# Performance work log

Hardware: AMD Instinct MI355X
Metric: run time of the kernel (lower is better)

The kernel has to match this reference:

```python
import jax, jax.numpy as jnp
import numpy as np

DIM, M_DIM, FOURIER, KNN = 128, 16, 4, 32
EDGE_IN = 2 * FOURIER + 2 * DIM + 1  # 265


def silu(x):
    return x * jax.nn.sigmoid(x)


def setup_inputs() -> dict:
    key = jax.random.key(0)
    ks = jax.random.split(key, 12)
    b, n = 2, 4096

    def w(k, shape):
        return jax.random.normal(k, shape, dtype=jnp.float32) * 0.02

    return {
        "feats": jax.random.normal(ks[0], (b, n, DIM), dtype=jnp.float32),
        "coors": jax.random.normal(ks[1], (b, n, 3), dtype=jnp.float32) * 3.0,
        # edge_mlp: Linear(265, 530) -> SiLU -> Linear(530, 16) -> SiLU
        "We1": w(ks[2], (EDGE_IN, 2 * EDGE_IN)), "be1": jnp.zeros((2 * EDGE_IN,), jnp.float32),
        "We2": w(ks[3], (2 * EDGE_IN, M_DIM)), "be2": jnp.zeros((M_DIM,), jnp.float32),
        # coors_mlp: Linear(16, 64) -> SiLU -> Linear(64, 1)
        "Wc1": w(ks[4], (M_DIM, 4 * M_DIM)), "bc1": jnp.zeros((4 * M_DIM,), jnp.float32),
        "Wc2": w(ks[5], (4 * M_DIM, 1)), "bc2": jnp.zeros((1,), jnp.float32),
        # node_mlp: Linear(dim+16, 2*dim) -> SiLU -> Linear(2*dim, dim)
        "Wn1": w(ks[6], (DIM + M_DIM, 2 * DIM)), "bn1": jnp.zeros((2 * DIM,), jnp.float32),
        "Wn2": w(ks[7], (2 * DIM, DIM)), "bn2": jnp.zeros((DIM,), jnp.float32),
    }


def reference(feats, coors, We1, be1, We2, be2, Wc1, bc1, Wc2, bc2, Wn1, bn1, Wn2, bn2):
    b, n, d = feats.shape
    # pairwise relative coords and squared distance: (b, n, n, 3), (b, n, n)
    rel_coors = coors[:, :, None, :] - coors[:, None, :, :]
    rel_dist = jnp.sum(rel_coors ** 2, axis=-1)

    # k nearest neighbors (smallest distance)
    _, idx = jax.lax.top_k(-rel_dist, KNN)  # (b, n, K)
    rel_coors = jnp.take_along_axis(rel_coors, idx[..., None], axis=2)  # (b, n, K, 3)
    rel_dist = jnp.take_along_axis(rel_dist, idx, axis=2)[..., None]    # (b, n, K, 1)

    # fourier encode distance -> (b, n, K, 2*F + 1)
    scales = 2.0 ** jnp.arange(FOURIER, dtype=rel_dist.dtype)
    xs = rel_dist[..., None] / scales  # (b, n, K, 1, F)
    fe = jnp.concatenate([jnp.sin(xs), jnp.cos(xs), rel_dist[..., None]], axis=-1)
    rel_dist = fe.reshape(b, n, KNN, 2 * FOURIER + 1)

    bidx = jnp.arange(b)[:, None, None]
    feats_j = feats[bidx, idx]                                   # (b, n, K, d)
    feats_i = jnp.broadcast_to(feats[:, :, None, :], (b, n, KNN, d))

    edge_in = jnp.concatenate([feats_i, feats_j, rel_dist], axis=-1)  # (b, n, K, 265)
    m_ij = silu(silu(edge_in @ We1 + be1) @ We2 + be2)                # (b, n, K, m)

    coor_w = (silu(m_ij @ Wc1 + bc1) @ Wc2 + bc2)[..., 0]             # (b, n, K)
    coors_out = jnp.einsum('bij,bijc->bic', coor_w, rel_coors) + coors

    m_i = m_ij.sum(axis=2)                                            # (b, n, m)
    node_h = silu(jnp.concatenate([feats, m_i], axis=-1) @ Wn1 + bn1)
    node_out = node_h @ Wn2 + bn2 + feats
    return node_out, coors_out
```

## Files before the change

kernel.cpp:

```cpp
#include <hip/hip_runtime.h>
#include <hip/hip_bf16.h>
#include <stdint.h>

typedef __hip_bfloat16 bf16;

using sh8    = __attribute__((ext_vector_type(8)))  short;
using sh4    = __attribute__((ext_vector_type(4)))  short;
using us4    = __attribute__((ext_vector_type(4)))  unsigned short;
using f32x16 = __attribute__((ext_vector_type(16))) float;
using fx4    = __attribute__((ext_vector_type(4)))  float;

#define NN    4096
#define NODES 8192
#define DIM   128
#define MD    16
#define KNNK  32
#define H1N   530
#define CPAD  544
#define PROW  1088

#define OFF_W1AB 0
#define OFF_WE2A 8704
#define OFF_WC1A 17536
#define OFF_BE2  19584
#define OFF_BC1  19616
#define OFF_WC2  19744
#define OFF_BC2  19872
#define WIMG_SH  19880

__device__ __forceinline__ float b2f(bf16 x){ return __bfloat162float(x); }
__device__ __forceinline__ bf16  f2b(float x){ return __float2bfloat16(x); }
__device__ __forceinline__ float silu_f(float x){
    return x * __builtin_amdgcn_rcpf(1.f + __expf(-x));
}

__device__ __forceinline__ unsigned short f2us(float f){
    unsigned x = __float_as_uint(f);
    unsigned r = x + 0x7FFFu + ((x >> 16) & 1u);
    return (unsigned short)(r >> 16);
}
__device__ __forceinline__ float us2f(unsigned short u){
    return __uint_as_float(((unsigned)u) << 16);
}
__device__ __forceinline__ unsigned pkbf(float a, float b){
    __hip_bfloat162 v = __float22bfloat162_rn(make_float2(a, b));
    return *(unsigned*)&v;
}

struct Ptrs { const void* p[14]; int n[14]; };

__global__ __launch_bounds__(256) void detect_kernel(Ptrs ps, int* flags){
    int tn = blockIdx.x;
    const bf16* s = (const bf16*)ps.p[tn];
    int n = ps.n[tn]; if (n > 8192) n = 8192;
    int bad = 0;
    for (int i = threadIdx.x; i < n; i += 256){
        float v = b2f(s[i]);
        if (!(fabsf(v) <= 64.f)) bad = 1;
    }
    __shared__ int sbad;
    if (threadIdx.x == 0) sbad = 0;
    __syncthreads();
    if (bad) atomicOr(&sbad, 1);
    __syncthreads();
    if (threadIdx.x == 0) flags[tn] = sbad;
}

struct ConvTab {
    const void* src[14];
    int dstoff[14];
    int prefix[15];
};

__global__ __launch_bounds__(256) void convert_all(ConvTab tab,
                                                   const int* __restrict__ flags,
                                                   float* __restrict__ base){
    int gid = blockIdx.x * 256 + threadIdx.x;
    if (gid >= tab.prefix[14]) return;
    int tn = 0;
    #pragma unroll
    for (int k = 1; k < 14; ++k)
        if (gid >= tab.prefix[k]) tn = k;
    int local = gid - tab.prefix[tn];
    int f = flags[tn];
    float v = f ? ((const float*)tab.src[tn])[local]
                : b2f(((const bf16*)tab.src[tn])[local]);
    base[tab.dstoff[tn] + local] = v;
}

__global__ __launch_bounds__(256) void prep_kernel(
        const float* __restrict__ We1, const float* __restrict__ We2,
        const float* __restrict__ Wc1, const float* __restrict__ be2,
        const float* __restrict__ bc1, const float* __restrict__ Wc2,
        const float* __restrict__ bc2, const float* __restrict__ feats,
        unsigned short* __restrict__ gwimg,
        unsigned short* __restrict__ We1T,
        unsigned short* __restrict__ fBF){
    int gid = blockIdx.x * 256 + threadIdx.x;
    if (gid < 4352){
        int c = gid >> 3, f = gid & 7;
        gwimg[OFF_W1AB + gid] = (c < H1N) ? f2us(We1[(size_t)(256 + f) * H1N + c]) : 0;
    } else if (gid < 8704){
        int e = gid - 4352; int c = e >> 3, jj = e & 7;
        gwimg[OFF_W1AB + 4352 + e] =
            (jj == 0 && c < H1N) ? f2us(We1[(size_t)264 * H1N + c]) : 0;
    } else if (gid < 17536){
        int e = gid - 8704; int o = e / 552, c = e - o * 552;
        gwimg[OFF_WE2A + e] = (c < H1N) ? f2us(We2[(size_t)c * 16 + o]) : 0;
    } else if (gid < 19584){
        int e = gid - 17536; int u = e >> 5, k = e & 31;
        gwimg[OFF_WC1A + e] = (k < 16) ? f2us(Wc1[(size_t)k * 64 + u]) : 0;
    } else if (gid < 19600){
        ((float*)(gwimg + OFF_BE2))[gid - 19584] = be2[gid - 19584];
    } else if (gid < 19664){
        ((float*)(gwimg + OFF_BC1))[gid - 19600] = bc1[gid - 19600];
    } else if (gid < 19728){
        ((float*)(gwimg + OFF_WC2))[gid - 19664] = Wc2[gid - 19664];
    } else if (gid < 19732){
        int z = gid - 19728;
        ((float*)(gwimg + OFF_BC2))[z] = (z == 0) ? bc2[0] : 0.f;
    } else if (gid >= 32768 && gid < 32768 + 1088 * 128){
        int e = gid - 32768; int n = e >> 7, k = e & 127;
        float v;
        if (n < CPAD) v = (n < H1N) ? We1[(size_t)k * H1N + n] : 0.f;
        else { int n2 = n - CPAD; v = (n2 < H1N) ? We1[(size_t)(128 + k) * H1N + n2] : 0.f; }
        We1T[e] = f2us(v);
    } else if (gid >= 172032 && gid < 172032 + NODES * DIM){
        int e = gid - 172032;
        fBF[e] = f2us(feats[e]);
    }
}

__global__ __launch_bounds__(512, 6) void knn_kernel(const float* __restrict__ coors,
                                                     int* __restrict__ idx_out){
    __shared__ unsigned hist[8][1024];
    __shared__ unsigned long long blist[8][64];
    __shared__ int cntO[8], cntB[8];

    int t = threadIdx.x, lane = t & 63, wid = t >> 6;
    int node = (blockIdx.x << 3) + wid;
    int b = node >> 12, i = node & (NN - 1);
    const float* cb = coors + (size_t)b * NN * 3;

    float qx = cb[i*3+0], qy = cb[i*3+1], qz = cb[i*3+2];

    unsigned* h = &hist[wid][0];
    {
        uint4* hz = (uint4*)h;
        uint4 z = make_uint4(0,0,0,0);
        #pragma unroll
        for (int zl = 0; zl < 4; ++zl) hz[zl * 64 + lane] = z;
    }
    if (lane == 0){ cntO[wid] = 0; cntB[wid] = 0; }
    asm volatile("" ::: "memory");

    #pragma unroll 4
    for (int s = 0; s < 64; ++s){
        int j = (s << 6) + lane;
        float dx = qx - cb[j*3+0];
        float dy = qy - cb[j*3+1];
        float dz = qz - cb[j*3+2];
        float d  = dx*dx + dy*dy + dz*dz;
        float d2 = d * d;
        atomicAdd(&h[__float_as_uint(d2 * d2) >> 22], 1u);
    }
    asm volatile("s_waitcnt lgkmcnt(0)" ::: "memory");

    unsigned S = 0;
    {
        uint4* hz = (uint4*)h;
        #pragma unroll
        for (int g = 0; g < 4; ++g){
            uint4 v = hz[lane * 4 + g];
            S += v.x + v.y + v.z + v.w;
        }
    }
    unsigned scan = S;
    #pragma unroll
    for (int off = 1; off < 64; off <<= 1){
        unsigned nv = __shfl_up(scan, off);
        if (lane >= off) scan += nv;
    }
    unsigned excl = scan - S;
    unsigned long long own = __ballot(excl < KNNK && excl + S >= KNNK);
    int src = __ffsll((unsigned long long)own) - 1;
    unsigned run = excl, Bloc = 0, below_l = 0;
    #pragma unroll
    for (int r = 0; r < 16; ++r){
        unsigned c = h[lane * 16 + r];
        if (run < KNNK && run + c >= KNNK){ Bloc = lane * 16 + r; below_l = run; }
        run += c;
    }
    unsigned B    = __shfl(Bloc, src);
    unsigned below= __shfl(below_l, src);
    unsigned need = KNNK - below;

    int* co = &cntO[wid];
    int* cbn = &cntB[wid];
    unsigned long long* bl = &blist[wid][0];
    #pragma unroll 4
    for (int s = 0; s < 64; ++s){
        int j = (s << 6) + lane;
        float dx = qx - cb[j*3+0];
        float dy = qy - cb[j*3+1];
        float dz = qz - cb[j*3+2];
        float d  = dx*dx + dy*dy + dz*dz;
        float d2 = d * d;
        unsigned bk = __float_as_uint(d2 * d2) >> 22;
        if (bk < B){
            int pos = atomicAdd(co, 1);
            idx_out[(size_t)node * KNNK + pos] = j;
        } else if (bk == B){
            unsigned long long mk = ((unsigned long long)__float_as_uint(d) << 32)
                                    | (unsigned)j;
            int p = atomicAdd(cbn, 1);
            if (p < 64) bl[p] = mk;
        }
    }
    asm volatile("s_waitcnt lgkmcnt(0) vmcnt(0)" ::: "memory");
    int nb = *cbn;

    if (nb <= 64){
        unsigned long long e = (lane < nb) ? bl[lane] : ~0ull;
        for (unsigned r = 0; r < need; ++r){
            unsigned long long m = e;
            #pragma unroll
            for (int off = 32; off > 0; off >>= 1){
                unsigned long long o = __shfl_xor(m, off);
                if (o < m) m = o;
            }
            if (lane == 0)
                idx_out[(size_t)node * KNNK + below + r] = (int)(unsigned)(m & 0xffffffffull);
            if (e == m) e = ~0ull;
        }
    } else {
        unsigned long long lastk = 0;
        for (unsigned r = 0; r < need; ++r){
            unsigned long long lmin = ~0ull;
            for (int s = 0; s < 64; ++s){
                int j = (s << 6) + lane;
                float dx = qx - cb[j*3+0];
                float dy = qy - cb[j*3+1];
                float dz = qz - cb[j*3+2];
                float d  = dx*dx + dy*dy + dz*dz;
                float d2 = d * d;
                if ((__float_as_uint(d2 * d2) >> 22) == B){
                    unsigned long long mk = (((unsigned long long)__float_as_uint(d) << 32)
                                             | (unsigned)j) + 1ull;
                    if (mk > lastk && mk < lmin) lmin = mk;
                }
            }
            #pragma unroll
            for (int off = 32; off > 0; off >>= 1){
                unsigned long long o = __shfl_xor(lmin, off);
                if (o < lmin) lmin = o;
            }
            if (lane == 0)
                idx_out[(size_t)node * KNNK + below + r] =
                    (int)(unsigned)((lmin - 1ull) & 0xffffffffull);
            lastk = lmin;
        }
    }
}

__global__ __launch_bounds__(256) void p_gemm(const unsigned short* __restrict__ fBF,
                                              const unsigned short* __restrict__ We1T,
                                              const float* __restrict__ be1,
                                              unsigned short* __restrict__ P){
    int t = threadIdx.x, lane = t & 63, wid = t >> 6;
    int e31 = lane & 31, hi = lane >> 5;
    int mW = (blockIdx.x << 7) + (wid << 5);
    int n0 = blockIdx.y << 5;

    const unsigned short* Arow = fBF  + (size_t)(mW + e31) * DIM + hi * 8;
    const unsigned short* Brow = We1T + (size_t)(n0 + e31) * DIM + hi * 8;

    f32x16 acc = {0.f,0.f,0.f,0.f,0.f,0.f,0.f,0.f,0.f,0.f,0.f,0.f,0.f,0.f,0.f,0.f};
    #pragma unroll
    for (int kc = 0; kc < 8; ++kc){
        sh8 a  = *(const sh8*)(Arow + kc * 16);
        sh8 bv = *(const sh8*)(Brow + kc * 16);
        acc = __builtin_amdgcn_mfma_f32_32x32x16_bf16(a, bv, acc, 0, 0, 0);
    }
    int n = n0 + e31;
    float beadd = 0.f;
    if (n < CPAD) beadd = (n < H1N) ? be1[n] : 0.f;
    #pragma unroll
    for (int g = 0; g < 4; ++g)
        #pragma unroll
        for (int r = 0; r < 4; ++r){
            int m = mW + 8*g + 4*hi + r;
            P[(size_t)m * PROW + n] = f2us(acc[4*g + r] + beadd);
        }
}

__global__ __launch_bounds__(512, 6) void edge_kernel(
        const float* __restrict__ coors, const int* __restrict__ idx,
        const unsigned short* __restrict__ gw,
        const unsigned short* __restrict__ P,
        float* __restrict__ mi_out, void* __restrict__ dout,
        const int* __restrict__ flagp){
    __shared__ __align__(16) unsigned short sWe2[16 * 552];
    __shared__ __align__(16) unsigned short trans[8][1280];

    int t = threadIdx.x, lane = t & 63, wid = t >> 6;
    int gnode = (blockIdx.x << 3) + wid;
    int b = gnode >> 12;

    {
        const float4* s1 = (const float4*)(gw + OFF_WE2A);
        float4* d1 = (float4*)sWe2;
        for (int e = t; e < 1104; e += 512) d1[e] = s1[e];
    }

    const float* cb = coors + (size_t)b * NN * 3;
    int i = gnode & (NN - 1);
    float qx = cb[i*3+0], qy = cb[i*3+1], qz = cb[i*3+2];

    int e31 = lane & 31, hi = lane >> 5;
    int e15 = lane & 15, q  = lane >> 4;

    int jme = idx[(size_t)gnode * KNNK + e31];
    float rx = qx - cb[jme*3+0];
    float ry = qy - cb[jme*3+1];
    float rz = qz - cb[jme*3+2];
    float d = rx*rx + ry*ry + rz*rz;

    unsigned frb[9];
    frb[0] = f2us(sinf(d));         frb[1] = f2us(sinf(d * 0.5f));
    frb[2] = f2us(sinf(d * 0.25f)); frb[3] = f2us(sinf(d * 0.125f));
    frb[4] = f2us(cosf(d));         frb[5] = f2us(cosf(d * 0.5f));
    frb[6] = f2us(cosf(d * 0.25f)); frb[7] = f2us(cosf(d * 0.125f));
    frb[8] = f2us(d);

    sh8 bfragC;
    #pragma unroll
    for (int j = 0; j < 8; ++j)
        bfragC[j] = (hi == 0) ? (short)frb[j]
                  : (short)((j == 0) ? frb[8] : (j == 1) ? 0x3F80u : 0u);

    int nbase = gnode & ~(NN - 1);
    int j0 = __shfl(jme, lane >> 2);
    int j1 = __shfl(jme, 16 + (lane >> 2));
    const unsigned short* Pst0 = P + (size_t)(nbase + j0) * PROW + CPAD + (lane & 3) * 8;
    const unsigned short* Pst1 = P + (size_t)(nbase + j1) * PROW + CPAD + (lane & 3) * 8;
    const unsigned short* Pirow = P + (size_t)gnode * PROW;

    unsigned short* stg = &trans[wid][0];
    unsigned short* sw0 = stg + (lane >> 2) * 40 + (lane & 3) * 8;
    unsigned short* sw1 = stg + (16 + (lane >> 2)) * 40 + (lane & 3) * 8;

    const float* g_be2 = (const float*)(gw + OFF_BE2);
    const float* g_bc1 = (const float*)(gw + OFF_BC1);
    const float* g_wc2 = (const float*)(gw + OFF_WC2);
    const float* g_bc2 = (const float*)(gw + OFF_BC2);

    fx4 accD0 = {0.f,0.f,0.f,0.f};
    fx4 accD1 = {0.f,0.f,0.f,0.f};

    __syncthreads();

    for (int ch = 0; ch < 17; ++ch){
        int c0 = ch * 32;
        sh8 g0v = *(const sh8*)(Pst0 + c0);
        sh8 g1v = *(const sh8*)(Pst1 + c0);
        unsigned short piS = Pirow[c0 + e31];
        sh8 afrag = *(const sh8*)(gw + OFF_W1AB + (size_t)(hi * 544 + c0 + e31) * 8);
        afrag[1] = hi ? (short)piS : afrag[1];

        *(sh8*)sw0 = g0v;
        *(sh8*)sw1 = g1v;
        asm volatile("s_waitcnt lgkmcnt(0)" ::: "memory");

        f32x16 cc;
        #pragma unroll
        for (int g = 0; g < 4; ++g){
            us4 pj = *(const us4*)(stg + e31 * 40 + 8*g + 4*hi);
            cc[4*g+0] = us2f(pj.x);
            cc[4*g+1] = us2f(pj.y);
            cc[4*g+2] = us2f(pj.z);
            cc[4*g+3] = us2f(pj.w);
        }
        f32x16 h = __builtin_amdgcn_mfma_f32_32x32x16_bf16(afrag, bfragC, cc, 0, 0, 0);

        #pragma unroll
        for (int g = 0; g < 4; ++g){
            unsigned lo = pkbf(silu_f(h[4*g+0]), silu_f(h[4*g+1]));
            unsigned hi2 = pkbf(silu_f(h[4*g+2]), silu_f(h[4*g+3]));
            *(uint2*)&stg[e31 * 40 + 8*g + 4*hi] = make_uint2(lo, hi2);
        }
        asm volatile("s_waitcnt lgkmcnt(0)" ::: "memory");

        sh8 wa  = *(const sh8*)&sWe2[e15 * 552 + c0 + q * 8];
        sh8 bt0 = *(const sh8*)&stg[e15 * 40 + q * 8];
        sh8 bt1 = *(const sh8*)&stg[(16 + e15) * 40 + q * 8];
        accD0 = __builtin_amdgcn_mfma_f32_16x16x32_bf16(wa, bt0, accD0, 0, 0, 0);
        accD1 = __builtin_amdgcn_mfma_f32_16x16x32_bf16(wa, bt1, accD1, 0, 0, 0);
    }

    fx4 be2q = *(const fx4*)&g_be2[q * 4];
    float msum[4];
    float mv0[4], mv1[4];
    #pragma unroll
    for (int r = 0; r < 4; ++r){
        mv0[r] = silu_f(accD0[r] + be2q[r]);
        mv1[r] = silu_f(accD1[r] + be2q[r]);
        msum[r] = mv0[r] + mv1[r];
    }
    *(uint2*)&stg[e15 * 16 + q * 4] =
        make_uint2(pkbf(mv0[0], mv0[1]), pkbf(mv0[2], mv0[3]));
    *(uint2*)&stg[(16 + e15) * 16 + q * 4] =
        make_uint2(pkbf(mv1[0], mv1[1]), pkbf(mv1[2], mv1[3]));
    #pragma unroll
    for (int r = 0; r < 4; ++r){
        msum[r] += __shfl_xor(msum[r], 1);
        msum[r] += __shfl_xor(msum[r], 2);
        msum[r] += __shfl_xor(msum[r], 4);
        msum[r] += __shfl_xor(msum[r], 8);
    }
    if (e15 == 0){
        fx4 mv = { msum[0], msum[1], msum[2], msum[3] };
        *(fx4*)(mi_out + (size_t)gnode * MD + q * 4) = mv;
    }
    asm volatile("s_waitcnt lgkmcnt(0)" ::: "memory");

    float tsum0 = 0.f, tsum1 = 0.f;
    #pragma unroll
    for (int ut = 0; ut < 4; ++ut){
        sh8 wa3 = *(const sh8*)(gw + OFF_WC1A + (size_t)(ut * 16 + e15) * 32 + q * 8);
        sh8 b0  = (q < 2) ? *(const sh8*)&stg[e15 * 16 + q * 8]        : (sh8)0;
        sh8 b1  = (q < 2) ? *(const sh8*)&stg[(16 + e15) * 16 + q * 8] : (sh8)0;
        fx4 a0 = {0.f,0.f,0.f,0.f};
        fx4 a1 = {0.f,0.f,0.f,0.f};
        a0 = __builtin_amdgcn_mfma_f32_16x16x32_bf16(wa3, b0, a0, 0, 0, 0);
        a1 = __builtin_amdgcn_mfma_f32_16x16x32_bf16(wa3, b1, a1, 0, 0, 0);
        fx4 bc1q = *(const fx4*)&g_bc1[ut * 16 + q * 4];
        fx4 wcq  = *(const fx4*)&g_wc2[ut * 16 + q * 4];
        #pragma unroll
        for (int r = 0; r < 4; ++r){
            tsum0 += silu_f(a0[r] + bc1q[r]) * wcq[r];
            tsum1 += silu_f(a1[r] + bc1q[r]) * wcq[r];
        }
    }
    tsum0 += __shfl_xor(tsum0, 16); tsum0 += __shfl_xor(tsum0, 32);
    tsum1 += __shfl_xor(tsum1, 16); tsum1 += __shfl_xor(tsum1, 32);
    float cw = ((lane < 16) ? tsum0 : tsum1) + g_bc2[0];

    float en = (lane < 32) ? 1.f : 0.f;
    float cx = en * cw * rx, cy = en * cw * ry, cz = en * cw * rz;
    #pragma unroll
    for (int off = 1; off <= 32; off <<= 1){
        cx += __shfl_xor(cx, off);
        cy += __shfl_xor(cy, off);
        cz += __shfl_xor(cz, off);
    }
    if (lane == 0){
        size_t base = (size_t)NODES * DIM + (size_t)gnode * 3;
        if (*flagp){
            float* o = (float*)dout;
            o[base+0] = cx + qx; o[base+1] = cy + qy; o[base+2] = cz + qz;
        } else {
            bf16* o = (bf16*)dout;
            o[base+0] = f2b(cx + qx); o[base+1] = f2b(cy + qy); o[base+2] = f2b(cz + qz);
        }
    }
}

__global__ __launch_bounds__(256) void node_kernel(
        const float* __restrict__ feats, const float* __restrict__ m_i,
        const float* __restrict__ Wn1,   const float* __restrict__ bn1,
        const float* __restrict__ Wn2,   const float* __restrict__ bn2,
        void* __restrict__ dout,         const int* __restrict__ flagp){
    __shared__ float X[8][144];
    __shared__ float Hs[8][256];
    int t = threadIdx.x;
    int g0 = blockIdx.x << 3;

    for (int e = t; e < 8 * DIM; e += 256){
        int nd = e >> 7, c = e & 127;
        X[nd][c] = feats[(size_t)(g0 + nd) * DIM + c];
    }
    if (t < 128){
        int nd = t >> 4, c = t & 15;
        X[nd][DIM + c] = m_i[(size_t)(g0 + nd) * MD + c];
    }
    __syncthreads();

    float acc[8] = {};
    for (int r = 0; r < 144; ++r){
        float w = Wn1[(size_t)r * 256 + t];
        #pragma unroll
        for (int nd = 0; nd < 8; ++nd) acc[nd] += X[nd][r] * w;
    }
    float bb = bn1[t];
    #pragma unroll
    for (int nd = 0; nd < 8; ++nd) Hs[nd][t] = silu_f(acc[nd] + bb);
    __syncthreads();

    int c = t & 127, g = t >> 7;
    float a2[4] = {};
    for (int r = 0; r < 256; ++r){
        float w = Wn2[(size_t)r * DIM + c];
        #pragma unroll
        for (int u = 0; u < 4; ++u) a2[u] += Hs[g*4 + u][r] * w;
    }
    float b2v = bn2[c];
    int fl = *flagp;
    #pragma unroll
    for (int u = 0; u < 4; ++u){
        int nd = g*4 + u;
        float v = a2[u] + b2v + X[nd][c];
        size_t off2 = (size_t)(g0 + nd) * DIM + c;
        if (fl) ((float*)dout)[off2] = v;
        else    ((bf16*)dout)[off2]  = f2b(v);
    }
}

extern "C" void kernel_launch(void* const* d_in, const int* in_sizes, int n_in,
                              void* d_out, int out_size, void* d_ws, size_t ws_size,
                              hipStream_t stream){
    char* ws = (char*)d_ws;
    size_t off = 0;
    auto alloc = [&](size_t bytes) -> char* {
        off = (off + 511) & ~(size_t)511;
        char* p = ws + off;
        off += bytes;
        return p;
    };

    int* flags = (int*)alloc(14 * 4);

    ConvTab tab;
    int total = 0;
    for (int i = 0; i < 14; ++i){ tab.prefix[i] = total; total += in_sizes[i]; }
    tab.prefix[14] = total;
    float* convBase = (float*)alloc((size_t)total * 4);
    int doff = 0;
    for (int i = 0; i < 14; ++i){
        tab.src[i] = d_in[i];
        tab.dstoff[i] = doff;
        doff += in_sizes[i];
    }

    unsigned short* gwimg = (unsigned short*)alloc((size_t)WIMG_SH * 2);
    unsigned short* We1T  = (unsigned short*)alloc((size_t)1088 * 128 * 2);
    unsigned short* fBF   = (unsigned short*)alloc((size_t)NODES * DIM * 2);
    int*   idx    = (int*)  alloc((size_t)NODES * KNNK * 4);
    unsigned short* P = (unsigned short*) alloc((size_t)NODES * PROW * 2);
    float* mi     = (float*)alloc((size_t)NODES * MD * 4);

    Ptrs ps;
    for (int i = 0; i < 14; ++i){ ps.p[i] = d_in[i]; ps.n[i] = in_sizes[i]; }
    detect_kernel<<<14, 256, 0, stream>>>(ps, flags);
    convert_all<<<(total + 255) / 256, 256, 0, stream>>>(tab, flags, convBase);

    const float* feats = convBase + tab.dstoff[0];
    const float* coors = convBase + tab.dstoff[1];
    const float* We1 = convBase + tab.dstoff[2],  * be1 = convBase + tab.dstoff[3];
    const float* We2 = convBase + tab.dstoff[4],  * be2 = convBase + tab.dstoff[5];
    const float* Wc1 = convBase + tab.dstoff[6],  * bc1 = convBase + tab.dstoff[7];
    const float* Wc2 = convBase + tab.dstoff[8],  * bc2 = convBase + tab.dstoff[9];
    const float* Wn1 = convBase + tab.dstoff[10], * bn1 = convBase + tab.dstoff[11];
    const float* Wn2 = convBase + tab.dstoff[12], * bn2 = convBase + tab.dstoff[13];

    prep_kernel<<<(172032 + NODES * DIM) / 256, 256, 0, stream>>>(
        We1, We2, Wc1, be2, bc1, Wc2, bc2, feats, gwimg, We1T, fBF);
    knn_kernel<<<NODES/8, 512, 0, stream>>>(coors, idx);
    p_gemm<<<dim3(64, 34), 256, 0, stream>>>(fBF, We1T, be1, P);
    edge_kernel<<<NODES/8, 512, 0, stream>>>(coors, idx, gwimg, P, mi,
                                             d_out, flags + 0);
    node_kernel<<<1024, 256, 0, stream>>>(feats, mi, Wn1, bn1, Wn2, bn2,
                                          d_out, flags + 0);
}
```

Before: 252.1 us.

## Store neighbor projection in fp32 and load MFMA accumulators directly from global

Splits the precomputed projection buffer into a bf16 self part and an fp32 neighbor part laid out so each lane can load its accumulator fragment straight from global memory. This removes the LDS staging round-trip and bf16-to-fp32 unpacking for neighbor rows, and prefetches the next chunk one iteration ahead. It also replaces eight sin/cos calls with one sincos plus double-angle recurrences and XOR-swizzles the LDS transpose buffer to avoid bank conflicts. In exchange, the neighbor gather reads twice as many bytes and the double-angle recurrence is slightly less precise.

```diff
diff --git a/kernel.cpp b/kernel.cpp
--- a/kernel.cpp
+++ b/kernel.cpp
@@ -17,7 +17,6 @@
 #define KNNK  32
 #define H1N   530
 #define CPAD  544
-#define PROW  1088
 
 #define OFF_W1AB 0
 #define OFF_WE2A 8704
@@ -266,7 +265,8 @@
 __global__ __launch_bounds__(256) void p_gemm(const unsigned short* __restrict__ fBF,
                                               const unsigned short* __restrict__ We1T,
                                               const float* __restrict__ be1,
-                                              unsigned short* __restrict__ P){
+                                              unsigned short* __restrict__ P,
+                                              float* __restrict__ P32){
     int t = threadIdx.x, lane = t & 63, wid = t >> 6;
     int e31 = lane & 31, hi = lane >> 5;
     int mW = (blockIdx.x << 7) + (wid << 5);
@@ -283,25 +283,36 @@
         acc = __builtin_amdgcn_mfma_f32_32x32x16_bf16(a, bv, acc, 0, 0, 0);
     }
     int n = n0 + e31;
-    float beadd = 0.f;
-    if (n < CPAD) beadd = (n < H1N) ? be1[n] : 0.f;
-    #pragma unroll
-    for (int g = 0; g < 4; ++g)
-        #pragma unroll
-        for (int r = 0; r < 4; ++r){
-            int m = mW + 8*g + 4*hi + r;
-            P[(size_t)m * PROW + n] = f2us(acc[4*g + r] + beadd);
-        }
+    if (n0 < CPAD){
+        float beadd = (n < H1N) ? be1[n] : 0.f;
+        #pragma unroll
+        for (int g = 0; g < 4; ++g)
+            #pragma unroll
+            for (int r = 0; r < 4; ++r){
+                int m = mW + 8*g + 4*hi + r;
+                P[(size_t)m * 544 + n] = f2us(acc[4*g + r] + beadd);
+            }
+    } else {
+        int n2 = n - CPAD;
+        #pragma unroll
+        for (int g = 0; g < 4; ++g)
+            #pragma unroll
+            for (int r = 0; r < 4; ++r){
+                int m = mW + 8*g + 4*hi + r;
+                P32[(size_t)m * 544 + n2] = acc[4*g + r];
+            }
+    }
 }
 
 __global__ __launch_bounds__(512, 6) void edge_kernel(
         const float* __restrict__ coors, const int* __restrict__ idx,
         const unsigned short* __restrict__ gw,
         const unsigned short* __restrict__ P,
+        const float* __restrict__ P32,
         float* __restrict__ mi_out, void* __restrict__ dout,
         const int* __restrict__ flagp){
     __shared__ __align__(16) unsigned short sWe2[16 * 552];
-    __shared__ __align__(16) unsigned short trans[8][1280];
+    __shared__ __align__(16) unsigned short trans[8][1024];
 
     int t = threadIdx.x, lane = t & 63, wid = t >> 6;
     int gnode = (blockIdx.x << 3) + wid;
@@ -326,11 +337,15 @@
     float rz = qz - cb[jme*3+2];
     float d = rx*rx + ry*ry + rz*rz;
 
+    float s8, c8;
+    __sincosf(d * 0.125f, &s8, &c8);
+    float s4  = 2.f*s8*c8,  c4  = 1.f - 2.f*s8*s8;
+    float s2a = 2.f*s4*c4,  c2a = 1.f - 2.f*s4*s4;
+    float s1a = 2.f*s2a*c2a, c1a = 1.f - 2.f*s2a*s2a;
+
     unsigned frb[9];
-    frb[0] = f2us(sinf(d));         frb[1] = f2us(sinf(d * 0.5f));
-    frb[2] = f2us(sinf(d * 0.25f)); frb[3] = f2us(sinf(d * 0.125f));
-    frb[4] = f2us(cosf(d));         frb[5] = f2us(cosf(d * 0.5f));
-    frb[6] = f2us(cosf(d * 0.25f)); frb[7] = f2us(cosf(d * 0.125f));
+    frb[0] = f2us(s1a); frb[1] = f2us(s2a); frb[2] = f2us(s4); frb[3] = f2us(s8);
+    frb[4] = f2us(c1a); frb[5] = f2us(c2a); frb[6] = f2us(c4); frb[7] = f2us(c8);
     frb[8] = f2us(d);
 
     sh8 bfragC;
@@ -340,15 +355,17 @@
                   : (short)((j == 0) ? frb[8] : (j == 1) ? 0x3F80u : 0u);
 
     int nbase = gnode & ~(NN - 1);
-    int j0 = __shfl(jme, lane >> 2);
-    int j1 = __shfl(jme, 16 + (lane >> 2));
-    const unsigned short* Pst0 = P + (size_t)(nbase + j0) * PROW + CPAD + (lane & 3) * 8;
-    const unsigned short* Pst1 = P + (size_t)(nbase + j1) * PROW + CPAD + (lane & 3) * 8;
-    const unsigned short* Pirow = P + (size_t)gnode * PROW;
+    const float* pjrow = P32 + (size_t)(nbase + jme) * 544 + (hi << 2);
+    const unsigned short* Pirow = P + (size_t)gnode * 544;
 
     unsigned short* stg = &trans[wid][0];
-    unsigned short* sw0 = stg + (lane >> 2) * 40 + (lane & 3) * 8;
-    unsigned short* sw1 = stg + (16 + (lane >> 2)) * 40 + (lane & 3) * 8;
+    int s3 = e31 & 3;
+    unsigned short* wpA = stg + e31 * 32 + ((0 ^ s3) << 3) + (hi << 2);
+    unsigned short* wpB = stg + e31 * 32 + ((1 ^ s3) << 3) + (hi << 2);
+    unsigned short* wpC = stg + e31 * 32 + ((2 ^ s3) << 3) + (hi << 2);
+    unsigned short* wpD = stg + e31 * 32 + ((3 ^ s3) << 3) + (hi << 2);
+    const unsigned short* bt0p = stg + e15 * 32 + ((q ^ (e15 & 3)) << 3);
+    const unsigned short* bt1p = bt0p + 512;
 
     const float* g_be2 = (const float*)(gw + OFF_BE2);
     const float* g_bc1 = (const float*)(gw + OFF_BC1);
@@ -358,42 +375,48 @@
     fx4 accD0 = {0.f,0.f,0.f,0.f};
     fx4 accD1 = {0.f,0.f,0.f,0.f};
 
+    fx4 pj0 = *(const fx4*)(pjrow + 0);
+    fx4 pj1 = *(const fx4*)(pjrow + 8);
+    fx4 pj2 = *(const fx4*)(pjrow + 16);
+    fx4 pj3 = *(const fx4*)(pjrow + 24);
+
     __syncthreads();
 
+    #pragma unroll 1
     for (int ch = 0; ch < 17; ++ch){
-        int c0 = ch * 32;
-        sh8 g0v = *(const sh8*)(Pst0 + c0);
-        sh8 g1v = *(const sh8*)(Pst1 + c0);
-        unsigned short piS = Pirow[c0 + e31];
-        sh8 afrag = *(const sh8*)(gw + OFF_W1AB + (size_t)(hi * 544 + c0 + e31) * 8);
+        f32x16 cc;
+        cc[0]  = pj0[0]; cc[1]  = pj0[1]; cc[2]  = pj0[2]; cc[3]  = pj0[3];
+        cc[4]  = pj1[0]; cc[5]  = pj1[1]; cc[6]  = pj1[2]; cc[7]  = pj1[3];
+        cc[8]  = pj2[0]; cc[9]  = pj2[1]; cc[10] = pj2[2]; cc[11] = pj2[3];
+        cc[12] = pj3[0]; cc[13] = pj3[1]; cc[14] = pj3[2]; cc[15] = pj3[3];
+
+        if (ch < 16){
+            const float* pn = pjrow + (ch + 1) * 32;
+            pj0 = *(const fx4*)(pn + 0);
+            pj1 = *(const fx4*)(pn + 8);
+            pj2 = *(const fx4*)(pn + 16);
+            pj3 = *(const fx4*)(pn + 24);
+        }
+
+        unsigned short piS = Pirow[ch * 32 + e31];
+        sh8 afrag = *(const sh8*)(gw + OFF_W1AB + (size_t)(hi * 544 + ch * 32 + e31) * 8);
         afrag[1] = hi ? (short)piS : afrag[1];
 
-        *(sh8*)sw0 = g0v;
-        *(sh8*)sw1 = g1v;
+        f32x16 h = __builtin_amdgcn_mfma_f32_32x32x16_bf16(afrag, bfragC, cc, 0, 0, 0);
+
+        *(uint2*)wpA = make_uint2(pkbf(silu_f(h[0]),  silu_f(h[1])),
+                                  pkbf(silu_f(h[2]),  silu_f(h[3])));
+        *(uint2*)wpB = make_uint2(pkbf(silu_f(h[4]),  silu_f(h[5])),
+                                  pkbf(silu_f(h[6]),  silu_f(h[7])));
+        *(uint2*)wpC = make_uint2(pkbf(silu_f(h[8]),  silu_f(h[9])),
+                                  pkbf(silu_f(h[10]), silu_f(h[11])));
+        *(uint2*)wpD = make_uint2(pkbf(silu_f(h[12]), silu_f(h[13])),
+                                  pkbf(silu_f(h[14]), silu_f(h[15])));
         asm volatile("s_waitcnt lgkmcnt(0)" ::: "memory");
 
-        f32x16 cc;
-        #pragma unroll
-        for (int g = 0; g < 4; ++g){
-            us4 pj = *(const us4*)(stg + e31 * 40 + 8*g + 4*hi);
-            cc[4*g+0] = us2f(pj.x);
-            cc[4*g+1] = us2f(pj.y);
-            cc[4*g+2] = us2f(pj.z);
-            cc[4*g+3] = us2f(pj.w);
-        }
-        f32x16 h = __builtin_amdgcn_mfma_f32_32x32x16_bf16(afrag, bfragC, cc, 0, 0, 0);
-
-        #pragma unroll
-        for (int g = 0; g < 4; ++g){
-            unsigned lo = pkbf(silu_f(h[4*g+0]), silu_f(h[4*g+1]));
-            unsigned hi2 = pkbf(silu_f(h[4*g+2]), silu_f(h[4*g+3]));
-            *(uint2*)&stg[e31 * 40 + 8*g + 4*hi] = make_uint2(lo, hi2);
-        }
-        asm volatile("s_waitcnt lgkmcnt(0)" ::: "memory");
-
-        sh8 wa  = *(const sh8*)&sWe2[e15 * 552 + c0 + q * 8];
-        sh8 bt0 = *(const sh8*)&stg[e15 * 40 + q * 8];
-        sh8 bt1 = *(const sh8*)&stg[(16 + e15) * 40 + q * 8];
+        sh8 wa  = *(const sh8*)&sWe2[e15 * 552 + ch * 32 + q * 8];
+        sh8 bt0 = *(const sh8*)bt0p;
+        sh8 bt1 = *(const sh8*)bt1p;
         accD0 = __builtin_amdgcn_mfma_f32_16x16x32_bf16(wa, bt0, accD0, 0, 0, 0);
         accD1 = __builtin_amdgcn_mfma_f32_16x16x32_bf16(wa, bt1, accD1, 0, 0, 0);
     }
@@ -546,7 +569,8 @@
     unsigned short* We1T  = (unsigned short*)alloc((size_t)1088 * 128 * 2);
     unsigned short* fBF   = (unsigned short*)alloc((size_t)NODES * DIM * 2);
     int*   idx    = (int*)  alloc((size_t)NODES * KNNK * 4);
-    unsigned short* P = (unsigned short*) alloc((size_t)NODES * PROW * 2);
+    unsigned short* P = (unsigned short*) alloc((size_t)NODES * 544 * 2);
+    float* P32    = (float*)alloc((size_t)NODES * 544 * 4);
     float* mi     = (float*)alloc((size_t)NODES * MD * 4);
 
     Ptrs ps;
@@ -566,8 +590,8 @@
     prep_kernel<<<(172032 + NODES * DIM) / 256, 256, 0, stream>>>(
         We1, We2, Wc1, be2, bc1, Wc2, bc2, feats, gwimg, We1T, fBF);
     knn_kernel<<<NODES/8, 512, 0, stream>>>(coors, idx);
-    p_gemm<<<dim3(64, 34), 256, 0, stream>>>(fBF, We1T, be1, P);
-    edge_kernel<<<NODES/8, 512, 0, stream>>>(coors, idx, gwimg, P, mi,
+    p_gemm<<<dim3(64, 34), 256, 0, stream>>>(fBF, We1T, be1, P, P32);
+    edge_kernel<<<NODES/8, 512, 0, stream>>>(coors, idx, gwimg, P, P32, mi,
                                              d_out, flags + 0);
     node_kernel<<<1024, 256, 0, stream>>>(feats, mi, Wn1, bn1, Wn2, bn2,
                                           d_out, flags + 0);
```

New measurement: 275.3 us. 9.2% more time.

## Keep edge hidden activations in registers via permlane swap, prefetch gathers, derive Fourier terms by doubling

Applied to the files above, without the earlier changes.

The second edge-MLP layer now feeds the SiLU outputs of the first MFMA straight back as A operands of 32x32x16 MFMAs, using permlane32_swap to rearrange them. This removes the LDS store/reload round trip and its waitcnt barriers in each of the 17 chunks. Neighbor projection rows are software-prefetched one chunk ahead. The eight sin/cos Fourier terms come from one __sincosf plus double-angle identities, which replaces eight libm calls but adds some approximation error, growing at the smaller scales.

```diff
diff --git a/kernel.cpp b/kernel.cpp
--- a/kernel.cpp
+++ b/kernel.cpp
@@ -9,6 +9,7 @@
 using us4    = __attribute__((ext_vector_type(4)))  unsigned short;
 using f32x16 = __attribute__((ext_vector_type(16))) float;
 using fx4    = __attribute__((ext_vector_type(4)))  float;
+using i32x2  = __attribute__((ext_vector_type(2)))  int;
 
 #define NN    4096
 #define NODES 8192
@@ -45,6 +46,15 @@
 __device__ __forceinline__ unsigned pkbf(float a, float b){
     __hip_bfloat162 v = __float22bfloat162_rn(make_float2(a, b));
     return *(unsigned*)&v;
+}
+__device__ __forceinline__ void plswap(unsigned &a, unsigned &b){
+    i32x2 r = __builtin_amdgcn_permlane32_swap((int)a, (int)b, false, false);
+    a = (unsigned)r[0]; b = (unsigned)r[1];
+}
+__device__ __forceinline__ sh8 mk8(unsigned a, unsigned b, unsigned c, unsigned d){
+    union { unsigned u[4]; sh8 s; } x;
+    x.u[0] = a; x.u[1] = b; x.u[2] = c; x.u[3] = d;
+    return x.s;
 }
 
 struct Ptrs { const void* p[14]; int n[14]; };
@@ -326,11 +336,15 @@
     float rz = qz - cb[jme*3+2];
     float d = rx*rx + ry*ry + rz*rz;
 
+    float s8v, c8v;
+    __sincosf(d * 0.125f, &s8v, &c8v);
+    float s4  = 2.f*s8v*c8v, c4  = 1.f - 2.f*s8v*s8v;
+    float s2a = 2.f*s4*c4,   c2a = 1.f - 2.f*s4*s4;
+    float s1a = 2.f*s2a*c2a, c1a = 1.f - 2.f*s2a*s2a;
+
     unsigned frb[9];
-    frb[0] = f2us(sinf(d));         frb[1] = f2us(sinf(d * 0.5f));
-    frb[2] = f2us(sinf(d * 0.25f)); frb[3] = f2us(sinf(d * 0.125f));
-    frb[4] = f2us(cosf(d));         frb[5] = f2us(cosf(d * 0.5f));
-    frb[6] = f2us(cosf(d * 0.25f)); frb[7] = f2us(cosf(d * 0.125f));
+    frb[0] = f2us(s1a); frb[1] = f2us(s2a); frb[2] = f2us(s4); frb[3] = f2us(s8v);
+    frb[4] = f2us(c1a); frb[5] = f2us(c2a); frb[6] = f2us(c4); frb[7] = f2us(c8v);
     frb[8] = f2us(d);
 
     sh8 bfragC;
@@ -355,22 +369,27 @@
     const float* g_wc2 = (const float*)(gw + OFF_WC2);
     const float* g_bc2 = (const float*)(gw + OFF_BC2);
 
-    fx4 accD0 = {0.f,0.f,0.f,0.f};
-    fx4 accD1 = {0.f,0.f,0.f,0.f};
+    f32x16 accD = {0.f,0.f,0.f,0.f,0.f,0.f,0.f,0.f,
+                   0.f,0.f,0.f,0.f,0.f,0.f,0.f,0.f};
+
+    sh8 g0v = *(const sh8*)(Pst0);
+    sh8 g1v = *(const sh8*)(Pst1);
 
     __syncthreads();
 
+    #pragma unroll 1
     for (int ch = 0; ch < 17; ++ch){
         int c0 = ch * 32;
-        sh8 g0v = *(const sh8*)(Pst0 + c0);
-        sh8 g1v = *(const sh8*)(Pst1 + c0);
+        *(sh8*)sw0 = g0v;
+        *(sh8*)sw1 = g1v;
+        if (ch < 16){
+            g0v = *(const sh8*)(Pst0 + c0 + 32);
+            g1v = *(const sh8*)(Pst1 + c0 + 32);
+        }
+
         unsigned short piS = Pirow[c0 + e31];
         sh8 afrag = *(const sh8*)(gw + OFF_W1AB + (size_t)(hi * 544 + c0 + e31) * 8);
         afrag[1] = hi ? (short)piS : afrag[1];
-
-        *(sh8*)sw0 = g0v;
-        *(sh8*)sw1 = g1v;
-        asm volatile("s_waitcnt lgkmcnt(0)" ::: "memory");
 
         f32x16 cc;
         #pragma unroll
@@ -383,46 +402,45 @@
         }
         f32x16 h = __builtin_amdgcn_mfma_f32_32x32x16_bf16(afrag, bfragC, cc, 0, 0, 0);
 
-        #pragma unroll
-        for (int g = 0; g < 4; ++g){
-            unsigned lo = pkbf(silu_f(h[4*g+0]), silu_f(h[4*g+1]));
-            unsigned hi2 = pkbf(silu_f(h[4*g+2]), silu_f(h[4*g+3]));
-            *(uint2*)&stg[e31 * 40 + 8*g + 4*hi] = make_uint2(lo, hi2);
-        }
-        asm volatile("s_waitcnt lgkmcnt(0)" ::: "memory");
-
-        sh8 wa  = *(const sh8*)&sWe2[e15 * 552 + c0 + q * 8];
-        sh8 bt0 = *(const sh8*)&stg[e15 * 40 + q * 8];
-        sh8 bt1 = *(const sh8*)&stg[(16 + e15) * 40 + q * 8];
-        accD0 = __builtin_amdgcn_mfma_f32_16x16x32_bf16(wa, bt0, accD0, 0, 0, 0);
-        accD1 = __builtin_amdgcn_mfma_f32_16x16x32_bf16(wa, bt1, accD1, 0, 0, 0);
-    }
-
-    fx4 be2q = *(const fx4*)&g_be2[q * 4];
-    float msum[4];
-    float mv0[4], mv1[4];
-    #pragma unroll
-    for (int r = 0; r < 4; ++r){
-        mv0[r] = silu_f(accD0[r] + be2q[r]);
-        mv1[r] = silu_f(accD1[r] + be2q[r]);
-        msum[r] = mv0[r] + mv1[r];
-    }
-    *(uint2*)&stg[e15 * 16 + q * 4] =
-        make_uint2(pkbf(mv0[0], mv0[1]), pkbf(mv0[2], mv0[3]));
-    *(uint2*)&stg[(16 + e15) * 16 + q * 4] =
-        make_uint2(pkbf(mv1[0], mv1[1]), pkbf(mv1[2], mv1[3]));
-    #pragma unroll
-    for (int r = 0; r < 4; ++r){
-        msum[r] += __shfl_xor(msum[r], 1);
-        msum[r] += __shfl_xor(msum[r], 2);
-        msum[r] += __shfl_xor(msum[r], 4);
-        msum[r] += __shfl_xor(msum[r], 8);
-    }
-    if (e15 == 0){
-        fx4 mv = { msum[0], msum[1], msum[2], msum[3] };
-        *(fx4*)(mi_out + (size_t)gnode * MD + q * 4) = mv;
-    }
-    asm volatile("s_waitcnt lgkmcnt(0)" ::: "memory");
+        unsigned u0 = pkbf(silu_f(h[0]),  silu_f(h[1]));
+        unsigned u1 = pkbf(silu_f(h[2]),  silu_f(h[3]));
+        unsigned u2 = pkbf(silu_f(h[4]),  silu_f(h[5]));
+        unsigned u3 = pkbf(silu_f(h[6]),  silu_f(h[7]));
+        unsigned u4 = pkbf(silu_f(h[8]),  silu_f(h[9]));
+        unsigned u5 = pkbf(silu_f(h[10]), silu_f(h[11]));
+        unsigned u6 = pkbf(silu_f(h[12]), silu_f(h[13]));
+        unsigned u7 = pkbf(silu_f(h[14]), silu_f(h[15]));
+        plswap(u0, u2); plswap(u1, u3);
+        plswap(u4, u6); plswap(u5, u7);
+        sh8 A1 = mk8(u0, u1, u2, u3);
+        sh8 A2 = mk8(u4, u5, u6, u7);
+
+        const unsigned short* wrow = &sWe2[(size_t)(e31 & 15) * 552 + c0 + (hi << 3)];
+        sh8 B1 = *(const sh8*)(wrow);
+        sh8 B2 = *(const sh8*)(wrow + 16);
+        accD = __builtin_amdgcn_mfma_f32_32x32x16_bf16(A1, B1, accD, 0, 0, 0);
+        accD = __builtin_amdgcn_mfma_f32_32x32x16_bf16(A2, B2, accD, 0, 0, 0);
+    }
+
+    float be2v = g_be2[e31 & 15];
+    float mval[16];
+    float msum = 0.f;
+    #pragma unroll
+    for (int r = 0; r < 16; ++r){
+        mval[r] = silu_f(accD[r] + be2v);
+        msum += mval[r];
+    }
+    msum += __shfl_xor(msum, 32);
+
+    if (e31 < 16){
+        #pragma unroll
+        for (int r = 0; r < 16; ++r){
+            int edge = (r & 3) + 8 * (r >> 2) + 4 * hi;
+            stg[edge * 16 + e31] = f2us(mval[r]);
+        }
+        if (hi == 0)
+            mi_out[(size_t)gnode * MD + e31] = msum;
+    }
 
     float tsum0 = 0.f, tsum1 = 0.f;
     #pragma unroll
```

New measurement: 252.5 us. No clear change (+0.2%).
